# Performance work log

Hardware: AMD Instinct MI355X
Metric: run time of the kernel (lower is better)

## Reference

```python
import jax, jax.numpy as jnp
import numpy as np

NUM_GRAPHS = 64
HID = 6
NUM_CLASSES = 10
NUM_FEATS = 128


def setup_inputs() -> dict:
    key = jax.random.key(0)
    ks = jax.random.split(key, 20)
    N, E = 100000, 3200000
    x = jax.random.normal(ks[0], (N, NUM_FEATS), dtype=jnp.float32)
    edge_index = jax.random.randint(ks[1], (2, E), 0, N, dtype=jnp.int64)
    batch = jnp.sort(jax.random.randint(ks[2], (N,), 0, NUM_GRAPHS, dtype=jnp.int64))
    def glorot(k, fan_in, fan_out):
        lim = np.sqrt(6.0 / (fan_in + fan_out))
        return jax.random.uniform(k, (fan_in, fan_out), jnp.float32, -lim, lim)
    inp = {"x": x, "edge_index": edge_index, "batch": batch}
    dims = [(NUM_FEATS, HID)] + [(HID, HID)] * 5 + [(HID, NUM_CLASSES)]
    names = ["1", "2", "3", "4", "5", "6", "f"]
    for i, (nm, (fi, fo)) in enumerate(zip(names, dims)):
        inp["W" + nm] = glorot(ks[3 + i], fi, fo)
        inp["b" + nm] = jnp.zeros((fo,), jnp.float32)
    return inp


def _gcn_forward(x, edge_index, batch, Ws, bs):
    N = x.shape[0]
    loop = jnp.arange(N, dtype=edge_index.dtype)
    src = jnp.concatenate([edge_index[0], loop])  # self-loops appended
    dst = jnp.concatenate([edge_index[1], loop])
    deg = jax.ops.segment_sum(jnp.ones_like(dst, dtype=x.dtype), dst, num_segments=N)
    dinv = jnp.where(deg > 0, jax.lax.rsqrt(deg), 0.0)
    norm = dinv[src] * dinv[dst]  # [E+N]

    def conv(h, W, b):
        h = h @ W  # [N, out]
        agg = jax.ops.segment_sum(h[src] * norm[:, None], dst, num_segments=N)
        return agg + b

    h = x
    for W, b in zip(Ws, bs):
        h = jax.nn.relu(conv(h, W, b))

    # global mean pool over graphs
    sums = jax.ops.segment_sum(h, batch, num_segments=NUM_GRAPHS)
    cnts = jax.ops.segment_sum(jnp.ones((N,), h.dtype), batch, num_segments=NUM_GRAPHS)
    pooled = sums / jnp.maximum(cnts, 1.0)[:, None]
    return jax.nn.log_softmax(pooled, axis=1)


def reference(x, edge_index, batch, W1, b1, W2, b2, W3, b3, W4, b4, W5, b5, W6, b6, Wf, bf):
    Ws = [W1, W2, W3, W4, W5, W6, Wf]
    bs = [b1, b2, b3, b4, b5, b6, bf]
    return _gcn_forward(x, edge_index, batch, Ws, bs)
```

## Files before the change

kernel.cpp:

```cpp
#include <hip/hip_runtime.h>
#include <hip/hip_bf16.h>
#include <hip/hip_fp16.h>
#include <math.h>

#define NF     128
#define HID    6
#define NC     10
#define NG     64
#define SLOTS  64
#define OVFCAP 8192

#define BKT_SH    7
#define BKT_NODES 128
#define NBK_MAX   1024
#define EPB       4096
#define BCAP      5120
#define BOVFCAP   4096

__device__ __forceinline__ void addh2(__half2& a0, __half2& a1, __half2& a2, uint4 q) {
    const __half2* h = (const __half2*)&q;
    a0 = __hadd2(a0, h[0]);
    a1 = __hadd2(a1, h[1]);
    a2 = __hadd2(a2, h[2]);
}

__device__ __forceinline__ __half2 shfl_xor_h2(__half2 v, int m) {
    union { __half2 h; unsigned int u; } a;
    a.h = v;
    a.u = __shfl_xor(a.u, m);
    return a.h;
}

__device__ __forceinline__ uint4 packh(const float* v) {
    uint4 q;
    __half2* h = (__half2*)&q;
    h[0] = __floats2half2_rn(v[0], v[1]);
    h[1] = __floats2half2_rn(v[2], v[3]);
    h[2] = __floats2half2_rn(v[4], v[5]);
    h[3] = __floats2half2_rn(0.f, 0.f);
    return q;
}

__global__ __launch_bounds__(256) void bucket_scatter_kernel(
        const int* __restrict__ src, const int* __restrict__ dst, int E, int nbk,
        int* __restrict__ bucket_cursor, unsigned int* __restrict__ bucket_arr,
        int* __restrict__ bovf_meta, int2* __restrict__ bovf) {
    __shared__ int cntL[NBK_MAX];
    __shared__ int offs[NBK_MAX + 1];
    __shared__ int gb[NBK_MAX];
    __shared__ int wtot[4];
    __shared__ unsigned int stage[EPB];
    int tid = threadIdx.x;
    for (int k = tid; k < NBK_MAX; k += 256) cntL[k] = 0;
    __syncthreads();
    int e0 = blockIdx.x * EPB;
    int cnt_e = E - e0; if (cnt_e > EPB) cnt_e = EPB;
    int sreg[16], dreg[16], rank[16];
    if (cnt_e == EPB && (E & 3) == 0) {
        const int4* s4p = (const int4*)(src + e0);
        const int4* d4p = (const int4*)(dst + e0);
#pragma unroll
        for (int k = 0; k < 4; ++k) {
            int4 sv = s4p[k * 256 + tid];
            int4 dv = d4p[k * 256 + tid];
            sreg[4*k+0] = sv.x; sreg[4*k+1] = sv.y; sreg[4*k+2] = sv.z; sreg[4*k+3] = sv.w;
            dreg[4*k+0] = dv.x; dreg[4*k+1] = dv.y; dreg[4*k+2] = dv.z; dreg[4*k+3] = dv.w;
        }
#pragma unroll
        for (int k = 0; k < 16; ++k) rank[k] = atomicAdd(&cntL[dreg[k] >> BKT_SH], 1);
    } else {
#pragma unroll
        for (int k = 0; k < 16; ++k) {
            int e = e0 + k * 256 + tid;
            if (e < E) {
                dreg[k] = dst[e]; sreg[k] = src[e];
                rank[k] = atomicAdd(&cntL[dreg[k] >> BKT_SH], 1);
            } else dreg[k] = -1;
        }
    }
    __syncthreads();
    int base = tid * 4;
    int c0 = cntL[base], c1 = cntL[base + 1], c2 = cntL[base + 2], c3 = cntL[base + 3];
    int tsum = c0 + c1 + c2 + c3;
    int lane = tid & 63, wv = tid >> 6;
    int v = tsum;
#pragma unroll
    for (int off = 1; off < 64; off <<= 1) {
        int u = __shfl_up(v, off);
        if (lane >= off) v += u;
    }
    if (lane == 63) wtot[wv] = v;
    __syncthreads();
    int wbase = 0;
    for (int w = 0; w < wv; ++w) wbase += wtot[w];
    int ex = wbase + v - tsum;
    offs[base]     = ex;
    offs[base + 1] = ex + c0;
    offs[base + 2] = ex + c0 + c1;
    offs[base + 3] = ex + c0 + c1 + c2;
    if (tid == 0) offs[NBK_MAX] = cnt_e;
    for (int bb = tid; bb < nbk; bb += 256) {
        int c = cntL[bb];
        if (c > 0) gb[bb] = atomicAdd(&bucket_cursor[bb], c);
    }
    __syncthreads();
#pragma unroll
    for (int k = 0; k < 16; ++k) {
        int d = dreg[k];
        if (d < 0) continue;
        int b = d >> BKT_SH;
        stage[offs[b] + rank[k]] =
            (unsigned int)(d & (BKT_NODES - 1)) | ((unsigned int)sreg[k] << BKT_SH);
    }
    __syncthreads();
    for (int j = tid; j < cnt_e; j += 256) {
        unsigned int p = stage[j];
        int lo = 0, hi = NBK_MAX;
        while (hi - lo > 1) {
            int mid = (lo + hi) >> 1;
            if (offs[mid] <= j) lo = mid; else hi = mid;
        }
        int b = lo;
        int grel = gb[b] + (j - offs[b]);
        if (grel < BCAP) {
            bucket_arr[(size_t)b * BCAP + grel] = p;
        } else {
            int d = (b << BKT_SH) | (int)(p & (BKT_NODES - 1));
            int s = (int)(p >> BKT_SH);
            int p2 = atomicAdd(bovf_meta, 1);
            if (p2 < BOVFCAP) bovf[p2] = make_int2(d, s);
        }
    }
}

__global__ __launch_bounds__(256) void ell_build_kernel(
        const unsigned int* __restrict__ bucket_arr, const int* __restrict__ bucket_cursor,
        const int* __restrict__ bovf_meta, const int2* __restrict__ bovf,
        int* __restrict__ ell, int* __restrict__ cnt, float* __restrict__ dinv,
        int* __restrict__ ovf_meta, int* __restrict__ ovf_dst, int* __restrict__ ovf_src,
        int N) {
    __shared__ int ell_s[BKT_NODES * SLOTS];
    __shared__ int cur[BKT_NODES];
    int b = blockIdx.x;
    int tid = threadIdx.x;
    if (tid < BKT_NODES) cur[tid] = 0;
    for (int k = tid; k < BKT_NODES * SLOTS; k += 256) ell_s[k] = N;
    __syncthreads();
    int bc = bucket_cursor[b];
    if (bc > BCAP) bc = BCAP;
    const unsigned int* ba = bucket_arr + (size_t)b * BCAP;
    for (int j = tid; j < bc; j += 256) {
        unsigned int p = ba[j];
        int r = (int)(p & (BKT_NODES - 1));
        int s = (int)(p >> BKT_SH);
        int slot = atomicAdd(&cur[r], 1);
        if (slot < SLOTS) {
            ell_s[r * SLOTS + slot] = s;
        } else {
            int d = (b << BKT_SH) + r;
            int q = atomicAdd(ovf_meta, 1);
            if (q < OVFCAP) { ovf_dst[q] = d; ovf_src[q] = s; }
        }
    }
    int m = *bovf_meta;
    if (m > BOVFCAP) m = BOVFCAP;
    for (int t = tid; t < m; t += 256) {
        int2 e = bovf[t];
        if ((e.x >> BKT_SH) == b) {
            int r = e.x & (BKT_NODES - 1);
            int slot = atomicAdd(&cur[r], 1);
            if (slot < SLOTS) {
                ell_s[r * SLOTS + slot] = e.y;
            } else {
                int q = atomicAdd(ovf_meta, 1);
                if (q < OVFCAP) { ovf_dst[q] = e.x; ovf_src[q] = e.y; }
            }
        }
    }
    __syncthreads();
    int nid0 = b << BKT_SH;
    int rows = N - nid0; if (rows > BKT_NODES) rows = BKT_NODES;
    if (rows <= 0) return;
    int4* eg = (int4*)(ell + (size_t)nid0 * SLOTS);
    const int4* es = (const int4*)ell_s;
    for (int k = tid; k < rows * (SLOTS / 4); k += 256) {
        int r = k >> 4;
        int q = k & 15;
        int c = cur[r]; if (c > SLOTS) c = SLOTS;
        if (q * 4 < c) eg[k] = es[k];
    }
    for (int r = tid; r < rows; r += 256) {
        int deg = cur[r];
        cnt[nid0 + r] = deg;
        dinv[nid0 + r] = rsqrtf((float)deg + 1.0f);
    }
}

__global__ __launch_bounds__(256) void layer1_kernel(const float* __restrict__ x,
                                                     const float* __restrict__ W,
                                                     const float* __restrict__ dinv,
                                                     uint4* __restrict__ g16, int N) {
    __shared__ float sW[8 * 100];
    for (int idx = threadIdx.x; idx < NF * HID; idx += 256) {
        int s = idx / 96, r = idx % 96;
        int o = r / 16, j = r % 16;
        sW[s * 100 + o * 16 + j] = W[(s * 16 + j) * HID + o];
    }
    __syncthreads();
    int t = blockIdx.x * 256 + threadIdx.x;
    int i = t >> 3;
    int sub = t & 7;
    if (t == 0) g16[N] = make_uint4(0u, 0u, 0u, 0u);
    if (i >= N) return;
    const float4* xr = (const float4*)(x + (size_t)i * NF + sub * 16);
    float4 xv0 = xr[0], xv1 = xr[1], xv2 = xr[2], xv3 = xr[3];
    const float4* wr = (const float4*)(sW + sub * 100);
    float p[HID];
#pragma unroll
    for (int o = 0; o < HID; ++o) {
        float4 w0 = wr[o * 4 + 0], w1 = wr[o * 4 + 1], w2 = wr[o * 4 + 2], w3 = wr[o * 4 + 3];
        p[o] = xv0.x * w0.x + xv0.y * w0.y + xv0.z * w0.z + xv0.w * w0.w
             + xv1.x * w1.x + xv1.y * w1.y + xv1.z * w1.z + xv1.w * w1.w
             + xv2.x * w2.x + xv2.y * w2.y + xv2.z * w2.z + xv2.w * w2.w
             + xv3.x * w3.x + xv3.y * w3.y + xv3.z * w3.z + xv3.w * w3.w;
    }
#pragma unroll
    for (int m = 1; m < 8; m <<= 1) {
#pragma unroll
        for (int o = 0; o < HID; ++o) p[o] += __shfl_xor(p[o], m);
    }
    if (sub == 0) {
        float dv = dinv[i];
        float v[HID];
#pragma unroll
        for (int o = 0; o < HID; ++o) v[o] = dv * p[o];
        g16[i] = packh(v);
    }
}

__device__ __forceinline__ void gather8h(int ne, const int* __restrict__ er,
                                         const uint4* __restrict__ g16, int sub,
                                         __half2& a0, __half2& a1, __half2& a2) {
#pragma unroll
    for (int r = 0; r < SLOTS / 32; ++r) {
        int base = r * 32 + sub * 4;
        if (base < ne) {
            int4 q = *(const int4*)(er + base);
            uint4 v0 = g16[q.x];
            uint4 v1 = g16[q.y];
            uint4 v2 = g16[q.z];
            uint4 v3 = g16[q.w];
            addh2(a0, a1, a2, v0);
            addh2(a0, a1, a2, v1);
            addh2(a0, a1, a2, v2);
            addh2(a0, a1, a2, v3);
        }
    }
}

template<int PREP>
__global__ __launch_bounds__(256) void gcn_layer8_kernel(
        const int* __restrict__ cnt, const int* __restrict__ ell,
        const int* __restrict__ ovf_meta, const int* __restrict__ ovf_dst,
        const int* __restrict__ ovf_src, const float* __restrict__ dinv,
        const uint4* __restrict__ gin, uint4* __restrict__ gout,
        const float* __restrict__ W, const float* __restrict__ b, int N) {
    int t = blockIdx.x * 256 + threadIdx.x;
    int i = t >> 3;
    int sub = t & 7;
    if (t == 0) gout[N] = make_uint4(0u, 0u, 0u, 0u);
    if (i >= N) return;
    int n = cnt[i];
    int ne = n < SLOTS ? n : SLOTS;
    const int* er = ell + (size_t)i * SLOTS;
    __half2 a0 = __float2half2_rn(0.f), a1 = a0, a2 = a0;
    gather8h(ne, er, gin, sub, a0, a1, a2);
    if (sub == 0) addh2(a0, a1, a2, gin[i]);
    if (n > SLOTS && sub == 2) {
        int m = ovf_meta[0];
        m = m < OVFCAP ? m : OVFCAP;
        for (int tt = 0; tt < m; ++tt) {
            if (ovf_dst[tt] == i) addh2(a0, a1, a2, gin[ovf_src[tt]]);
        }
    }
#pragma unroll
    for (int m = 1; m < 8; m <<= 1) {
        a0 = __hadd2(a0, shfl_xor_h2(a0, m));
        a1 = __hadd2(a1, shfl_xor_h2(a1, m));
        a2 = __hadd2(a2, shfl_xor_h2(a2, m));
    }
    if (sub != 0) return;
    float2 f0 = __half22float2(a0), f1 = __half22float2(a1), f2 = __half22float2(a2);
    float acc[HID] = { f0.x, f0.y, f1.x, f1.y, f2.x, f2.y };
    float dv = dinv[i];
    float h[HID];
#pragma unroll
    for (int f = 0; f < HID; ++f) {
        float u = dv * acc[f] + b[f];
        h[f] = u > 0.0f ? u : 0.0f;
    }
    float o[HID];
    if (PREP) {
#pragma unroll
        for (int f = 0; f < HID; ++f) o[f] = dv * h[f];
    } else {
#pragma unroll
        for (int fo = 0; fo < HID; ++fo) {
            float s = 0.0f;
#pragma unroll
            for (int fi = 0; fi < HID; ++fi) s += h[fi] * W[fi * HID + fo];
            o[fo] = dv * s;
        }
    }
    gout[i] = packh(o);
}

__global__ __launch_bounds__(256) void pool_kernel(
        const int* __restrict__ cnt, const int* __restrict__ ell,
        const int* __restrict__ ovf_meta, const int* __restrict__ ovf_dst,
        const int* __restrict__ ovf_src, const float* __restrict__ dinv,
        const uint4* __restrict__ gin, const int* __restrict__ batch,
        const float* __restrict__ Wf, const float* __restrict__ bf,
        float* __restrict__ pooled, float* __restrict__ gcnt, int N) {
    __shared__ float sp[NG * NC];
    __shared__ float sc[NG];
    __shared__ int srange[2];
    for (int k = threadIdx.x; k < NG * NC; k += 256) sp[k] = 0.0f;
    if (threadIdx.x < NG) sc[threadIdx.x] = 0.0f;
    int start = blockIdx.x * 32;
    int endi = min(start + 32, N) - 1;
    if (threadIdx.x == 0) {
        srange[0] = batch[start];
        srange[1] = batch[endi];
    }
    __syncthreads();
    int t = blockIdx.x * 256 + threadIdx.x;
    int i = t >> 3;
    int sub = t & 7;
    if (i < N) {
        int n = cnt[i];
        int ne = n < SLOTS ? n : SLOTS;
        const int* er = ell + (size_t)i * SLOTS;
        __half2 a0 = __float2half2_rn(0.f), a1 = a0, a2 = a0;
        gather8h(ne, er, gin, sub, a0, a1, a2);
        if (sub == 0) addh2(a0, a1, a2, gin[i]);
        if (n > SLOTS && sub == 2) {
            int m = ovf_meta[0];
            m = m < OVFCAP ? m : OVFCAP;
            for (int tt = 0; tt < m; ++tt) {
                if (ovf_dst[tt] == i) addh2(a0, a1, a2, gin[ovf_src[tt]]);
            }
        }
#pragma unroll
        for (int m = 1; m < 8; m <<= 1) {
            a0 = __hadd2(a0, shfl_xor_h2(a0, m));
            a1 = __hadd2(a1, shfl_xor_h2(a1, m));
            a2 = __hadd2(a2, shfl_xor_h2(a2, m));
        }
        if (sub == 0) {
            float2 f0 = __half22float2(a0), f1 = __half22float2(a1), f2 = __half22float2(a2);
            float acc[HID] = { f0.x, f0.y, f1.x, f1.y, f2.x, f2.y };
            float dv = dinv[i];
            float u[HID];
#pragma unroll
            for (int f = 0; f < HID; ++f) u[f] = dv * acc[f];
            int bg = batch[i];
#pragma unroll
            for (int c = 0; c < NC; ++c) {
                float v = bf[c];
#pragma unroll
                for (int f = 0; f < HID; ++f) v += u[f] * Wf[f * NC + c];
                v = v > 0.0f ? v : 0.0f;
                atomicAdd(&sp[bg * NC + c], v);
            }
            atomicAdd(&sc[bg], 1.0f);
        }
    }
    __syncthreads();
    int bmin = srange[0], bmax = srange[1];
    int rows = bmax - bmin + 1;
    for (int k = threadIdx.x; k < rows * NC; k += 256) {
        int r = bmin + k / NC, c = k % NC;
        float v = sp[r * NC + c];
        if (v != 0.0f) atomicAdd(&pooled[r * NC + c], v);
    }
    for (int k = threadIdx.x; k < rows; k += 256) {
        float v = sc[bmin + k];
        if (v != 0.0f) atomicAdd(&gcnt[bmin + k], v);
    }
}

__global__ void logsm_kernel(const float* __restrict__ pooled, const float* __restrict__ gcnt,
                             float* __restrict__ out) {
    int gidx = threadIdx.x;
    if (gidx >= NG) return;
    float c = gcnt[gidx];
    c = c > 1.0f ? c : 1.0f;
    float v[NC];
    float m = -1e30f;
#pragma unroll
    for (int k = 0; k < NC; ++k) {
        v[k] = pooled[gidx * NC + k] / c;
        m = v[k] > m ? v[k] : m;
    }
    float s = 0.0f;
#pragma unroll
    for (int k = 0; k < NC; ++k) s += expf(v[k] - m);
    float ls = logf(s);
#pragma unroll
    for (int k = 0; k < NC; ++k) out[gidx * NC + k] = v[k] - m - ls;
}

extern "C" void kernel_launch(void* const* d_in, const int* in_sizes, int n_in,
                              void* d_out, int out_size, void* d_ws, size_t ws_size,
                              hipStream_t stream) {
    const float* x     = (const float*)d_in[0];
    const int*   ei    = (const int*)d_in[1];
    const int*   batch = (const int*)d_in[2];
    const float* W[7];
    const float* b[7];
    for (int l = 0; l < 7; ++l) {
        W[l] = (const float*)d_in[3 + 2 * l];
        b[l] = (const float*)d_in[4 + 2 * l];
    }
    const int N = in_sizes[2];
    const int E = in_sizes[1] / 2;
    const int nbk = (N + BKT_NODES - 1) >> BKT_SH;
    const int* src = ei;
    const int* dst = ei + E;
    float* out = (float*)d_out;

    char* wp = (char*)d_ws;
    int* bucket_cursor = (int*)wp;  wp += (size_t)NBK_MAX * 4;
    int* ovf_meta  = (int*)wp;      wp += 16;
    int* bovf_meta = (int*)wp;      wp += 16;
    int* ovf_dst   = (int*)wp;      wp += OVFCAP * 4;
    int* ovf_src   = (int*)wp;      wp += OVFCAP * 4;
    int2* bovf     = (int2*)wp;     wp += (size_t)BOVFCAP * 8;
    int* cnt       = (int*)wp;      wp += (((size_t)N * 4 + 15) & ~15ull);
    float* dinv    = (float*)wp;    wp += (((size_t)N * 4 + 15) & ~15ull);
    uint4* g_a     = (uint4*)wp;    wp += (size_t)(N + 1) * 16;
    uint4* g_b     = (uint4*)wp;    wp += (size_t)(N + 1) * 16;
    float* pooled  = (float*)wp;    wp += NG * NC * 4;
    float* gcnt    = (float*)wp;    wp += (((size_t)NG * 4 + 15) & ~15ull);
    int* ell       = (int*)wp;      wp += (size_t)N * SLOTS * 4;
    unsigned int* bucket_arr = (unsigned int*)wp;  wp += (size_t)nbk * BCAP * 4;

    hipMemsetAsync(bucket_cursor, 0, (size_t)NBK_MAX * 4 + 32, stream);
    hipMemsetAsync(pooled, 0, (NG * NC + NG) * sizeof(float), stream);

    const int BT = 256;
    int bn8 = ((size_t)N * 8 + BT - 1) / BT;
    int bp1 = (E + EPB - 1) / EPB;

    bucket_scatter_kernel<<<bp1, BT, 0, stream>>>(src, dst, E, nbk, bucket_cursor,
                                                  bucket_arr, bovf_meta, bovf);
    ell_build_kernel<<<nbk, BT, 0, stream>>>(bucket_arr, bucket_cursor, bovf_meta, bovf,
                                             ell, cnt, dinv, ovf_meta, ovf_dst, ovf_src, N);

    layer1_kernel<<<bn8, BT, 0, stream>>>(x, W[0], dinv, g_a, N);

    gcn_layer8_kernel<0><<<bn8, BT, 0, stream>>>(cnt, ell, ovf_meta, ovf_dst, ovf_src, dinv, g_a, g_b, W[1], b[0], N);
    gcn_layer8_kernel<0><<<bn8, BT, 0, stream>>>(cnt, ell, ovf_meta, ovf_dst, ovf_src, dinv, g_b, g_a, W[2], b[1], N);
    gcn_layer8_kernel<0><<<bn8, BT, 0, stream>>>(cnt, ell, ovf_meta, ovf_dst, ovf_src, dinv, g_a, g_b, W[3], b[2], N);
    gcn_layer8_kernel<0><<<bn8, BT, 0, stream>>>(cnt, ell, ovf_meta, ovf_dst, ovf_src, dinv, g_b, g_a, W[4], b[3], N);
    gcn_layer8_kernel<0><<<bn8, BT, 0, stream>>>(cnt, ell, ovf_meta, ovf_dst, ovf_src, dinv, g_a, g_b, W[5], b[4], N);
    gcn_layer8_kernel<1><<<bn8, BT, 0, stream>>>(cnt, ell, ovf_meta, ovf_dst, ovf_src, dinv, g_b, g_a, nullptr, b[5], N);
    pool_kernel<<<bn8, BT, 0, stream>>>(cnt, ell, ovf_meta, ovf_dst, ovf_src, dinv, g_a, batch, W[6], b[6], pooled, gcnt, N);
    logsm_kernel<<<1, 64, 0, stream>>>(pooled, gcnt, out);
}
```

Baseline: 345.3 us.

## Coarsen scatter buckets to 512 nodes and split ELL build into sub-buckets

Bucket scatter now groups edges into 256 buckets of 512 destination nodes instead of 1024 buckets of 128. This simplifies the per-block scan to one counter per thread and cuts global atomics and scattered small writes. The ELL build launches four blocks per coarse bucket, and each block rereads the whole bucket and keeps only its 128-node quarter. The trade is fewer, larger scatter segments against four times the bucket read traffic in the build kernel.

Result: slower. 353.8 us (+2.5%).

```diff
diff --git a/kernel.cpp b/kernel.cpp
--- a/kernel.cpp
+++ b/kernel.cpp
@@ -10,11 +10,13 @@
 #define SLOTS  64
 #define OVFCAP 8192
 
-#define BKT_SH    7
-#define BKT_NODES 128
-#define NBK_MAX   1024
+#define BKT_SH    9
+#define BKT_NODES 512
+#define NBK_MAX   256
+#define SUB_SH    7
+#define SUB_NODES 128
 #define EPB       4096
-#define BCAP      5120
+#define BCAP      18432
 #define BOVFCAP   4096
 
 __device__ __forceinline__ void addh2(__half2& a0, __half2& a1, __half2& a2, uint4 q) {
@@ -51,7 +53,7 @@
     __shared__ int wtot[4];
     __shared__ unsigned int stage[EPB];
     int tid = threadIdx.x;
-    for (int k = tid; k < NBK_MAX; k += 256) cntL[k] = 0;
+    if (tid < NBK_MAX) cntL[tid] = 0;
     __syncthreads();
     int e0 = blockIdx.x * EPB;
     int cnt_e = E - e0; if (cnt_e > EPB) cnt_e = EPB;
@@ -79,11 +81,9 @@
         }
     }
     __syncthreads();
-    int base = tid * 4;
-    int c0 = cntL[base], c1 = cntL[base + 1], c2 = cntL[base + 2], c3 = cntL[base + 3];
-    int tsum = c0 + c1 + c2 + c3;
     int lane = tid & 63, wv = tid >> 6;
-    int v = tsum;
+    int c = cntL[tid];
+    int v = c;
 #pragma unroll
     for (int off = 1; off < 64; off <<= 1) {
         int u = __shfl_up(v, off);
@@ -93,16 +93,10 @@
     __syncthreads();
     int wbase = 0;
     for (int w = 0; w < wv; ++w) wbase += wtot[w];
-    int ex = wbase + v - tsum;
-    offs[base]     = ex;
-    offs[base + 1] = ex + c0;
-    offs[base + 2] = ex + c0 + c1;
-    offs[base + 3] = ex + c0 + c1 + c2;
+    int ex = wbase + v - c;
+    offs[tid] = ex;
     if (tid == 0) offs[NBK_MAX] = cnt_e;
-    for (int bb = tid; bb < nbk; bb += 256) {
-        int c = cntL[bb];
-        if (c > 0) gb[bb] = atomicAdd(&bucket_cursor[bb], c);
-    }
+    if (tid < nbk && c > 0) gb[tid] = atomicAdd(&bucket_cursor[tid], c);
     __syncthreads();
 #pragma unroll
     for (int k = 0; k < 16; ++k) {
@@ -139,25 +133,30 @@
         int* __restrict__ ell, int* __restrict__ cnt, float* __restrict__ dinv,
         int* __restrict__ ovf_meta, int* __restrict__ ovf_dst, int* __restrict__ ovf_src,
         int N) {
-    __shared__ int ell_s[BKT_NODES * SLOTS];
-    __shared__ int cur[BKT_NODES];
+    __shared__ int ell_s[SUB_NODES * SLOTS];
+    __shared__ int cur[SUB_NODES];
     int b = blockIdx.x;
+    int pb = b >> 2;
+    int subq = b & 3;
     int tid = threadIdx.x;
-    if (tid < BKT_NODES) cur[tid] = 0;
-    for (int k = tid; k < BKT_NODES * SLOTS; k += 256) ell_s[k] = N;
-    __syncthreads();
-    int bc = bucket_cursor[b];
+    if (tid < SUB_NODES) cur[tid] = 0;
+    for (int k = tid; k < SUB_NODES * SLOTS; k += 256) ell_s[k] = N;
+    __syncthreads();
+    int bc = bucket_cursor[pb];
     if (bc > BCAP) bc = BCAP;
-    const unsigned int* ba = bucket_arr + (size_t)b * BCAP;
+    const unsigned int* ba = bucket_arr + (size_t)pb * BCAP;
+    int rlo = subq << SUB_SH;
     for (int j = tid; j < bc; j += 256) {
         unsigned int p = ba[j];
         int r = (int)(p & (BKT_NODES - 1));
+        if ((r >> SUB_SH) != subq) continue;
         int s = (int)(p >> BKT_SH);
-        int slot = atomicAdd(&cur[r], 1);
+        int rl = r & (SUB_NODES - 1);
+        int slot = atomicAdd(&cur[rl], 1);
         if (slot < SLOTS) {
-            ell_s[r * SLOTS + slot] = s;
+            ell_s[rl * SLOTS + slot] = s;
         } else {
-            int d = (b << BKT_SH) + r;
+            int d = (b << SUB_SH) + rl;
             int q = atomicAdd(ovf_meta, 1);
             if (q < OVFCAP) { ovf_dst[q] = d; ovf_src[q] = s; }
         }
@@ -166,11 +165,11 @@
     if (m > BOVFCAP) m = BOVFCAP;
     for (int t = tid; t < m; t += 256) {
         int2 e = bovf[t];
-        if ((e.x >> BKT_SH) == b) {
-            int r = e.x & (BKT_NODES - 1);
-            int slot = atomicAdd(&cur[r], 1);
+        if ((e.x >> SUB_SH) == b) {
+            int rl = e.x & (SUB_NODES - 1);
+            int slot = atomicAdd(&cur[rl], 1);
             if (slot < SLOTS) {
-                ell_s[r * SLOTS + slot] = e.y;
+                ell_s[rl * SLOTS + slot] = e.y;
             } else {
                 int q = atomicAdd(ovf_meta, 1);
                 if (q < OVFCAP) { ovf_dst[q] = e.x; ovf_src[q] = e.y; }
@@ -178,8 +177,8 @@
         }
     }
     __syncthreads();
-    int nid0 = b << BKT_SH;
-    int rows = N - nid0; if (rows > BKT_NODES) rows = BKT_NODES;
+    int nid0 = b << SUB_SH;
+    int rows = N - nid0; if (rows > SUB_NODES) rows = SUB_NODES;
     if (rows <= 0) return;
     int4* eg = (int4*)(ell + (size_t)nid0 * SLOTS);
     const int4* es = (const int4*)ell_s;
@@ -425,7 +424,8 @@
     }
     const int N = in_sizes[2];
     const int E = in_sizes[1] / 2;
-    const int nbk = (N + BKT_NODES - 1) >> BKT_SH;
+    const int nbk  = (N + BKT_NODES - 1) >> BKT_SH;
+    const int nsub = (N + SUB_NODES - 1) >> SUB_SH;
     const int* src = ei;
     const int* dst = ei + E;
     float* out = (float*)d_out;
@@ -455,8 +455,8 @@
 
     bucket_scatter_kernel<<<bp1, BT, 0, stream>>>(src, dst, E, nbk, bucket_cursor,
                                                   bucket_arr, bovf_meta, bovf);
-    ell_build_kernel<<<nbk, BT, 0, stream>>>(bucket_arr, bucket_cursor, bovf_meta, bovf,
-                                             ell, cnt, dinv, ovf_meta, ovf_dst, ovf_src, N);
+    ell_build_kernel<<<nsub, BT, 0, stream>>>(bucket_arr, bucket_cursor, bovf_meta, bovf,
+                                              ell, cnt, dinv, ovf_meta, ovf_dst, ovf_src, N);
 
     layer1_kernel<<<bn8, BT, 0, stream>>>(x, W[0], dinv, g_a, N);
 
```

## Fuse six GCN layers, pooling and log-softmax into one cooperative persistent kernel

Applied to the files above, without the earlier changes.

Replaces the eight per-layer, pool and log-softmax launches with a single cooperative kernel of 512 blocks that keeps each node's ELL neighbor indices, degree and dinv in registers across all layers. Layers are separated by grid-wide syncs, and the final log-softmax runs after a last grid sync. The aim is to remove launch overhead and repeated ELL index loads per layer. In exchange it adds grid-sync latency and register pressure from holding 8 chunks of indices per thread, and it keeps the old kernels as a fallback if the cooperative launch fails. The pool kernel's flush is also simplified to push all graph slots instead of a per-block batch range.

Measured after the change: 817.9 us. 137% more time.

```diff
diff --git a/kernel.cpp b/kernel.cpp
--- a/kernel.cpp
+++ b/kernel.cpp
@@ -1,7 +1,10 @@
 #include <hip/hip_runtime.h>
 #include <hip/hip_bf16.h>
 #include <hip/hip_fp16.h>
+#include <hip/hip_cooperative_groups.h>
 #include <math.h>
+
+namespace cg = cooperative_groups;
 
 #define NF     128
 #define HID    6
@@ -16,6 +19,14 @@
 #define EPB       4096
 #define BCAP      5120
 #define BOVFCAP   4096
+
+#define GRID_F 512
+#define CH     8
+
+struct LayerParams {
+    const float* W[7];
+    const float* b[7];
+};
 
 __device__ __forceinline__ void addh2(__half2& a0, __half2& a1, __half2& a2, uint4 q) {
     const __half2* h = (const __half2*)&q;
@@ -324,15 +335,8 @@
         float* __restrict__ pooled, float* __restrict__ gcnt, int N) {
     __shared__ float sp[NG * NC];
     __shared__ float sc[NG];
-    __shared__ int srange[2];
     for (int k = threadIdx.x; k < NG * NC; k += 256) sp[k] = 0.0f;
     if (threadIdx.x < NG) sc[threadIdx.x] = 0.0f;
-    int start = blockIdx.x * 32;
-    int endi = min(start + 32, N) - 1;
-    if (threadIdx.x == 0) {
-        srange[0] = batch[start];
-        srange[1] = batch[endi];
-    }
     __syncthreads();
     int t = blockIdx.x * 256 + threadIdx.x;
     int i = t >> 3;
@@ -377,16 +381,13 @@
         }
     }
     __syncthreads();
-    int bmin = srange[0], bmax = srange[1];
-    int rows = bmax - bmin + 1;
-    for (int k = threadIdx.x; k < rows * NC; k += 256) {
-        int r = bmin + k / NC, c = k % NC;
-        float v = sp[r * NC + c];
-        if (v != 0.0f) atomicAdd(&pooled[r * NC + c], v);
-    }
-    for (int k = threadIdx.x; k < rows; k += 256) {
-        float v = sc[bmin + k];
-        if (v != 0.0f) atomicAdd(&gcnt[bmin + k], v);
+    for (int k = threadIdx.x; k < NG * NC; k += 256) {
+        float v = sp[k];
+        if (v != 0.0f) atomicAdd(&pooled[k], v);
+    }
+    if (threadIdx.x < NG) {
+        float v = sc[threadIdx.x];
+        if (v != 0.0f) atomicAdd(&gcnt[threadIdx.x], v);
     }
 }
 
@@ -411,17 +412,203 @@
     for (int k = 0; k < NC; ++k) out[gidx * NC + k] = v[k] - m - ls;
 }
 
+__global__ __launch_bounds__(256, 2) void gcn_fused_kernel(
+        const int* __restrict__ cnt, const int* __restrict__ ell,
+        const int* __restrict__ ovf_meta, const int* __restrict__ ovf_dst,
+        const int* __restrict__ ovf_src, const float* __restrict__ dinv,
+        uint4* __restrict__ g_a, uint4* __restrict__ g_b,
+        const int* __restrict__ batch, float* __restrict__ pooled,
+        float* __restrict__ gcntp, float* __restrict__ out, LayerParams P, int N) {
+    cg::grid_group grid = cg::this_grid();
+    __shared__ float sp[NG * NC];
+    __shared__ float sc[NG];
+    int tid = threadIdx.x;
+    int sub = tid & 7;
+    int lrow = tid >> 3;
+    int G = (N + 31) >> 5;
+
+    int  ii[CH]; int nn[CH]; float dd[CH]; bool act[CH];
+    int4 q0[CH], q1[CH];
+#pragma unroll
+    for (int c = 0; c < CH; ++c) {
+        int grp = blockIdx.x + c * GRID_F;
+        int i = grp * 32 + lrow;
+        act[c] = (grp < G) && (i < N);
+        ii[c] = act[c] ? i : 0;
+        q0[c] = make_int4(N, N, N, N); q1[c] = q0[c];
+        nn[c] = 0; dd[c] = 0.f;
+        if (act[c]) {
+            int n = cnt[i];
+            nn[c] = n;
+            dd[c] = dinv[i];
+            const int4* er = (const int4*)(ell + (size_t)i * SLOTS);
+            int ne = n < SLOTS ? n : SLOTS;
+            if (sub * 4 < ne)      q0[c] = er[sub];
+            if (32 + sub * 4 < ne) q1[c] = er[8 + sub];
+        }
+    }
+
+#pragma unroll
+    for (int l = 0; l < 6; ++l) {
+        const uint4* gin = (l & 1) ? g_b : g_a;
+        uint4*       gout = (l & 1) ? g_a : g_b;
+#pragma unroll
+        for (int c = 0; c < CH; ++c) {
+            if (!act[c]) continue;
+            int n = nn[c];
+            int ne = n < SLOTS ? n : SLOTS;
+            __half2 a0 = __float2half2_rn(0.f), a1 = a0, a2 = a0;
+            if (sub * 4 < ne) {
+                int4 q = q0[c];
+                uint4 v0 = gin[q.x], v1 = gin[q.y], v2 = gin[q.z], v3 = gin[q.w];
+                addh2(a0, a1, a2, v0); addh2(a0, a1, a2, v1);
+                addh2(a0, a1, a2, v2); addh2(a0, a1, a2, v3);
+            }
+            if (32 + sub * 4 < ne) {
+                int4 q = q1[c];
+                uint4 v0 = gin[q.x], v1 = gin[q.y], v2 = gin[q.z], v3 = gin[q.w];
+                addh2(a0, a1, a2, v0); addh2(a0, a1, a2, v1);
+                addh2(a0, a1, a2, v2); addh2(a0, a1, a2, v3);
+            }
+            if (sub == 0) addh2(a0, a1, a2, gin[ii[c]]);
+            if (n > SLOTS && sub == 2) {
+                int m = ovf_meta[0];
+                m = m < OVFCAP ? m : OVFCAP;
+                for (int tt = 0; tt < m; ++tt) {
+                    if (ovf_dst[tt] == ii[c]) addh2(a0, a1, a2, gin[ovf_src[tt]]);
+                }
+            }
+#pragma unroll
+            for (int m = 1; m < 8; m <<= 1) {
+                a0 = __hadd2(a0, shfl_xor_h2(a0, m));
+                a1 = __hadd2(a1, shfl_xor_h2(a1, m));
+                a2 = __hadd2(a2, shfl_xor_h2(a2, m));
+            }
+            if (sub == 0) {
+                float2 f0 = __half22float2(a0), f1 = __half22float2(a1), f2 = __half22float2(a2);
+                float acc[HID] = { f0.x, f0.y, f1.x, f1.y, f2.x, f2.y };
+                float dv = dd[c];
+                float h[HID];
+#pragma unroll
+                for (int f = 0; f < HID; ++f) {
+                    float u = dv * acc[f] + P.b[l][f];
+                    h[f] = u > 0.0f ? u : 0.0f;
+                }
+                float o[HID];
+                if (l == 5) {
+#pragma unroll
+                    for (int f = 0; f < HID; ++f) o[f] = dv * h[f];
+                } else {
+                    const float* Wn = P.W[l + 1];
+#pragma unroll
+                    for (int fo = 0; fo < HID; ++fo) {
+                        float s = 0.0f;
+#pragma unroll
+                        for (int fi = 0; fi < HID; ++fi) s += h[fi] * Wn[fi * HID + fo];
+                        o[fo] = dv * s;
+                    }
+                }
+                gout[ii[c]] = packh(o);
+            }
+        }
+        grid.sync();
+    }
+
+    for (int k = tid; k < NG * NC; k += 256) sp[k] = 0.0f;
+    if (tid < NG) sc[tid] = 0.0f;
+    __syncthreads();
+    const uint4* gin = g_a;
+#pragma unroll
+    for (int c = 0; c < CH; ++c) {
+        if (!act[c]) continue;
+        int n = nn[c];
+        int ne = n < SLOTS ? n : SLOTS;
+        __half2 a0 = __float2half2_rn(0.f), a1 = a0, a2 = a0;
+        if (sub * 4 < ne) {
+            int4 q = q0[c];
+            uint4 v0 = gin[q.x], v1 = gin[q.y], v2 = gin[q.z], v3 = gin[q.w];
+            addh2(a0, a1, a2, v0); addh2(a0, a1, a2, v1);
+            addh2(a0, a1, a2, v2); addh2(a0, a1, a2, v3);
+        }
+        if (32 + sub * 4 < ne) {
+            int4 q = q1[c];
+            uint4 v0 = gin[q.x], v1 = gin[q.y], v2 = gin[q.z], v3 = gin[q.w];
+            addh2(a0, a1, a2, v0); addh2(a0, a1, a2, v1);
+            addh2(a0, a1, a2, v2); addh2(a0, a1, a2, v3);
+        }
+        if (sub == 0) addh2(a0, a1, a2, gin[ii[c]]);
+        if (n > SLOTS && sub == 2) {
+            int m = ovf_meta[0];
+            m = m < OVFCAP ? m : OVFCAP;
+            for (int tt = 0; tt < m; ++tt) {
+                if (ovf_dst[tt] == ii[c]) addh2(a0, a1, a2, gin[ovf_src[tt]]);
+            }
+        }
+#pragma unroll
+        for (int m = 1; m < 8; m <<= 1) {
+            a0 = __hadd2(a0, shfl_xor_h2(a0, m));
+            a1 = __hadd2(a1, shfl_xor_h2(a1, m));
+            a2 = __hadd2(a2, shfl_xor_h2(a2, m));
+        }
+        if (sub == 0) {
+            float2 f0 = __half22float2(a0), f1 = __half22float2(a1), f2 = __half22float2(a2);
+            float acc[HID] = { f0.x, f0.y, f1.x, f1.y, f2.x, f2.y };
+            float dv = dd[c];
+            float u[HID];
+#pragma unroll
+            for (int f = 0; f < HID; ++f) u[f] = dv * acc[f];
+            int bg = batch[ii[c]];
+#pragma unroll
+            for (int cc = 0; cc < NC; ++cc) {
+                float v = P.b[6][cc];
+#pragma unroll
+                for (int f = 0; f < HID; ++f) v += u[f] * P.W[6][f * NC + cc];
+                v = v > 0.0f ? v : 0.0f;
+                atomicAdd(&sp[bg * NC + cc], v);
+            }
+            atomicAdd(&sc[bg], 1.0f);
+        }
+    }
+    __syncthreads();
+    for (int k = tid; k < NG * NC; k += 256) {
+        float v = sp[k];
+        if (v != 0.0f) atomicAdd(&pooled[k], v);
+    }
+    if (tid < NG) {
+        float v = sc[tid];
+        if (v != 0.0f) atomicAdd(&gcntp[tid], v);
+    }
+    grid.sync();
+
+    if (blockIdx.x == 0 && tid < NG) {
+        float c = gcntp[tid];
+        c = c > 1.0f ? c : 1.0f;
+        float v[NC];
+        float m = -1e30f;
+#pragma unroll
+        for (int k = 0; k < NC; ++k) {
+            v[k] = pooled[tid * NC + k] / c;
+            m = v[k] > m ? v[k] : m;
+        }
+        float s = 0.0f;
+#pragma unroll
+        for (int k = 0; k < NC; ++k) s += expf(v[k] - m);
+        float ls = logf(s);
+#pragma unroll
+        for (int k = 0; k < NC; ++k) out[tid * NC + k] = v[k] - m - ls;
+    }
+}
+
 extern "C" void kernel_launch(void* const* d_in, const int* in_sizes, int n_in,
                               void* d_out, int out_size, void* d_ws, size_t ws_size,
                               hipStream_t stream) {
     const float* x     = (const float*)d_in[0];
     const int*   ei    = (const int*)d_in[1];
     const int*   batch = (const int*)d_in[2];
-    const float* W[7];
-    const float* b[7];
+    LayerParams P;
     for (int l = 0; l < 7; ++l) {
-        W[l] = (const float*)d_in[3 + 2 * l];
-        b[l] = (const float*)d_in[4 + 2 * l];
+        P.W[l] = (const float*)d_in[3 + 2 * l];
+        P.b[l] = (const float*)d_in[4 + 2 * l];
     }
     const int N = in_sizes[2];
     const int E = in_sizes[1] / 2;
@@ -442,12 +629,13 @@
     uint4* g_a     = (uint4*)wp;    wp += (size_t)(N + 1) * 16;
     uint4* g_b     = (uint4*)wp;    wp += (size_t)(N + 1) * 16;
     float* pooled  = (float*)wp;    wp += NG * NC * 4;
-    float* gcnt    = (float*)wp;    wp += (((size_t)NG * 4 + 15) & ~15ull);
+    float* gcntp   = (float*)wp;    wp += (((size_t)NG * 4 + 15) & ~15ull);
     int* ell       = (int*)wp;      wp += (size_t)N * SLOTS * 4;
     unsigned int* bucket_arr = (unsigned int*)wp;  wp += (size_t)nbk * BCAP * 4;
 
     hipMemsetAsync(bucket_cursor, 0, (size_t)NBK_MAX * 4 + 32, stream);
     hipMemsetAsync(pooled, 0, (NG * NC + NG) * sizeof(float), stream);
+    hipMemsetAsync(g_b + N, 0, 16, stream);
 
     const int BT = 256;
     int bn8 = ((size_t)N * 8 + BT - 1) / BT;
@@ -458,14 +646,22 @@
     ell_build_kernel<<<nbk, BT, 0, stream>>>(bucket_arr, bucket_cursor, bovf_meta, bovf,
                                              ell, cnt, dinv, ovf_meta, ovf_dst, ovf_src, N);
 
-    layer1_kernel<<<bn8, BT, 0, stream>>>(x, W[0], dinv, g_a, N);
-
-    gcn_layer8_kernel<0><<<bn8, BT, 0, stream>>>(cnt, ell, ovf_meta, ovf_dst, ovf_src, dinv, g_a, g_b, W[1], b[0], N);
-    gcn_layer8_kernel<0><<<bn8, BT, 0, stream>>>(cnt, ell, ovf_meta, ovf_dst, ovf_src, dinv, g_b, g_a, W[2], b[1], N);
-    gcn_layer8_kernel<0><<<bn8, BT, 0, stream>>>(cnt, ell, ovf_meta, ovf_dst, ovf_src, dinv, g_a, g_b, W[3], b[2], N);
-    gcn_layer8_kernel<0><<<bn8, BT, 0, stream>>>(cnt, ell, ovf_meta, ovf_dst, ovf_src, dinv, g_b, g_a, W[4], b[3], N);
-    gcn_layer8_kernel<0><<<bn8, BT, 0, stream>>>(cnt, ell, ovf_meta, ovf_dst, ovf_src, dinv, g_a, g_b, W[5], b[4], N);
-    gcn_layer8_kernel<1><<<bn8, BT, 0, stream>>>(cnt, ell, ovf_meta, ovf_dst, ovf_src, dinv, g_b, g_a, nullptr, b[5], N);
-    pool_kernel<<<bn8, BT, 0, stream>>>(cnt, ell, ovf_meta, ovf_dst, ovf_src, dinv, g_a, batch, W[6], b[6], pooled, gcnt, N);
-    logsm_kernel<<<1, 64, 0, stream>>>(pooled, gcnt, out);
-}
+    layer1_kernel<<<bn8, BT, 0, stream>>>(x, P.W[0], dinv, g_a, N);
+
+    void* kargs[] = { (void*)&cnt, (void*)&ell, (void*)&ovf_meta, (void*)&ovf_dst,
+                      (void*)&ovf_src, (void*)&dinv, (void*)&g_a, (void*)&g_b,
+                      (void*)&batch, (void*)&pooled, (void*)&gcntp, (void*)&out,
+                      (void*)&P, (void*)&N };
+    hipError_t cerr = hipLaunchCooperativeKernel((void*)gcn_fused_kernel, dim3(GRID_F),
+                                                 dim3(BT), kargs, 0, stream);
+    if (cerr != hipSuccess) {
+        gcn_layer8_kernel<0><<<bn8, BT, 0, stream>>>(cnt, ell, ovf_meta, ovf_dst, ovf_src, dinv, g_a, g_b, P.W[1], P.b[0], N);
+        gcn_layer8_kernel<0><<<bn8, BT, 0, stream>>>(cnt, ell, ovf_meta, ovf_dst, ovf_src, dinv, g_b, g_a, P.W[2], P.b[1], N);
+        gcn_layer8_kernel<0><<<bn8, BT, 0, stream>>>(cnt, ell, ovf_meta, ovf_dst, ovf_src, dinv, g_a, g_b, P.W[3], P.b[2], N);
+        gcn_layer8_kernel<0><<<bn8, BT, 0, stream>>>(cnt, ell, ovf_meta, ovf_dst, ovf_src, dinv, g_b, g_a, P.W[4], P.b[3], N);
+        gcn_layer8_kernel<0><<<bn8, BT, 0, stream>>>(cnt, ell, ovf_meta, ovf_dst, ovf_src, dinv, g_a, g_b, P.W[5], P.b[4], N);
+        gcn_layer8_kernel<1><<<bn8, BT, 0, stream>>>(cnt, ell, ovf_meta, ovf_dst, ovf_src, dinv, g_b, g_a, nullptr, P.b[5], N);
+        pool_kernel<<<bn8, BT, 0, stream>>>(cnt, ell, ovf_meta, ovf_dst, ovf_src, dinv, g_a, batch, P.W[6], P.b[6], pooled, gcntp, N);
+        logsm_kernel<<<1, 64, 0, stream>>>(pooled, gcntp, out);
+    }
+}
```
